# Performance work log

Measured on AMD Instinct MI355X. Metric: run time of the kernel, lower is better.

Reference implementation:

```python
import jax, jax.numpy as jnp
import numpy as np

NUM_SLOTS = 8
DIM = 256
ITERS = 3
EPS_LN = 1e-5

def _ln(x, g, b):
    mu = jnp.mean(x, axis=-1, keepdims=True)
    var = jnp.var(x, axis=-1, keepdims=True)
    return (x - mu) * jax.lax.rsqrt(var + EPS_LN) * g + b

def setup_inputs() -> dict:
    key = jax.random.key(0)
    ks = jax.random.split(key, 16)
    d = DIM
    s = 1.0 / np.sqrt(d)
    inp = {
        'x': jax.random.normal(ks[0], (64, 4096, d), jnp.float32),
        'noise': jax.random.normal(ks[1], (64, NUM_SLOTS, d), jnp.float32),
        'slots_mu': jax.random.normal(ks[2], (1, 1, d), jnp.float32),
        'slots_logsigma': jnp.zeros((1, 1, d), jnp.float32),
        'Wq': jax.random.uniform(ks[3], (d, d), jnp.float32, -s, s),
        'Wk': jax.random.uniform(ks[4], (d, d), jnp.float32, -s, s),
        'Wv': jax.random.uniform(ks[5], (d, d), jnp.float32, -s, s),
        'W_ih': jax.random.uniform(ks[6], (3 * d, d), jnp.float32, -s, s),
        'W_hh': jax.random.uniform(ks[7], (3 * d, d), jnp.float32, -s, s),
        'b_ih': jax.random.uniform(ks[8], (3 * d,), jnp.float32, -s, s),
        'b_hh': jax.random.uniform(ks[9], (3 * d,), jnp.float32, -s, s),
        'W1': jax.random.uniform(ks[10], (d, d), jnp.float32, -s, s),
        'b1': jax.random.uniform(ks[11], (d,), jnp.float32, -s, s),
        'W2': jax.random.uniform(ks[12], (d, d), jnp.float32, -s, s),
        'b2': jax.random.uniform(ks[13], (d,), jnp.float32, -s, s),
        'g_in': jnp.ones((d,), jnp.float32), 'be_in': jnp.zeros((d,), jnp.float32),
        'g_sl': jnp.ones((d,), jnp.float32), 'be_sl': jnp.zeros((d,), jnp.float32),
        'g_ff': jnp.ones((d,), jnp.float32), 'be_ff': jnp.zeros((d,), jnp.float32),
    }
    return inp

def _gru(x, h, W_ih, W_hh, b_ih, b_hh):
    # torch.nn.GRUCell math; x,h: [M, d]
    gi = x @ W_ih.T + b_ih
    gh = h @ W_hh.T + b_hh
    i_r, i_z, i_n = jnp.split(gi, 3, axis=-1)
    h_r, h_z, h_n = jnp.split(gh, 3, axis=-1)
    r = jax.nn.sigmoid(i_r + h_r)
    z = jax.nn.sigmoid(i_z + h_z)
    n = jnp.tanh(i_n + r * h_n)
    return (1.0 - z) * n + z * h

def reference(x, noise, slots_mu, slots_logsigma, Wq, Wk, Wv, W_ih, W_hh, b_ih, b_hh,
              W1, b1, W2, b2, g_in, be_in, g_sl, be_sl, g_ff, be_ff):
    B, N, d = x.shape
    scale = d ** (-0.5)
    x = _ln(x, g_in, be_in)
    slots = slots_mu + noise * jnp.exp(slots_logsigma)  # [B, K, d]
    # k/v are loop-invariant; hoist (same math as original)
    k = jnp.einsum('bnd,ed->bne', x, Wk)
    v = jnp.einsum('bnd,ed->bne', x, Wv)
    for _ in range(ITERS):
        slots_prev = slots
        q = jnp.einsum('bkd,ed->bke', _ln(slots, g_sl, be_sl), Wq)
        attn = jax.nn.softmax(jnp.einsum('bkd,bnd->bkn', q, k) * scale, axis=-1) + 1e-8
        attn = attn / jnp.sum(attn, axis=-1, keepdims=True)
        updates = jnp.einsum('bkn,bnd->bkd', attn, v)
        slots = _gru(updates.reshape(-1, d), slots_prev.reshape(-1, d),
                     W_ih, W_hh, b_ih, b_hh).reshape(B, NUM_SLOTS, d)
        h = jax.nn.relu(jnp.einsum('bkd,ed->bke', _ln(slots, g_ff, be_ff), W1) + b1)
        slots = slots + jnp.einsum('bkd,ed->bke', h, W2) + b2
    return slots.reshape(B, NUM_SLOTS * d)
```

## Files before the change

### kernel.cpp

```cpp
#include <hip/hip_runtime.h>
#include <cstddef>

#define DIM 256
#define NSLOT 8
#define BATCH 64
#define NTOK 4096
#define SEGB 16
#define NPART SEGB
#define ITERS 3
#define EPS 1e-5f

typedef short bf16x8 __attribute__((ext_vector_type(8)));
typedef short bf16x4 __attribute__((ext_vector_type(4)));
typedef float f32x4  __attribute__((ext_vector_type(4)));

static __device__ __forceinline__ short f2bf(float f) {
    union { float f; unsigned u; } v; v.f = f;
    unsigned r = v.u + 0x7fffu + ((v.u >> 16) & 1u);
    return (short)(r >> 16);
}

enum : size_t {
    OFF_M     = 0,
    OFF_WIHT  = OFF_M    + 256 * 256,
    OFF_WHHT  = OFF_WIHT + 256 * 768,
    OFF_WVT   = OFF_WHHT + 256 * 768,
    OFF_W1T   = OFF_WVT  + 256 * 256,
    OFF_W2T   = OFF_W1T  + 256 * 256,
    OFF_SLOTS = OFF_W2T  + 256 * 256,
    OFF_SNEW  = OFF_SLOTS + BATCH * NSLOT * 256,
    OFF_QT    = OFF_SNEW  + BATCH * NSLOT * 256,
    OFF_H     = OFF_QT    + BATCH * NSLOT * 256,
    OFF_UPD   = OFF_H     + BATCH * NSLOT * 256,
    OFF_UPART = OFF_UPD   + BATCH * NSLOT * 256,
    OFF_LPART = OFF_UPART + (size_t)BATCH * NPART * NSLOT * 256,
    WS_FLOATS = OFF_LPART + BATCH * NPART * 16
};

__global__ __launch_bounds__(256) void k_transpose(const float* __restrict__ w_ih,
                                                   const float* __restrict__ w_hh,
                                                   const float* __restrict__ wv,
                                                   const float* __restrict__ w1,
                                                   const float* __restrict__ w2,
                                                   float* __restrict__ ws) {
    int z = blockIdx.z;
    const float* src;
    float* dst;
    int R;
    if (z == 0)      { src = w_ih; dst = ws + OFF_WIHT; R = 768; }
    else if (z == 1) { src = w_hh; dst = ws + OFF_WHHT; R = 768; }
    else if (z == 2) { src = wv;   dst = ws + OFF_WVT;  R = 256; }
    else if (z == 3) { src = w1;   dst = ws + OFF_W1T;  R = 256; }
    else             { src = w2;   dst = ws + OFF_W2T;  R = 256; }
    if ((int)blockIdx.x * 32 >= R) return;
    __shared__ float tile[32][33];
    int lx = threadIdx.x & 31, ly = threadIdx.x >> 5;
    int r0 = blockIdx.x * 32, c0 = blockIdx.y * 32;
#pragma unroll
    for (int p = 0; p < 4; ++p)
        tile[ly + p * 8][lx] = src[(size_t)(r0 + ly + p * 8) * 256 + c0 + lx];
    __syncthreads();
#pragma unroll
    for (int p = 0; p < 4; ++p)
        dst[(size_t)(c0 + ly + p * 8) * R + r0 + lx] = tile[lx][ly + p * 8];
}

__global__ __launch_bounds__(256) void k_m(const float* __restrict__ wq,
                                           const float* __restrict__ wk,
                                           float* __restrict__ ws) {
    int d = blockIdx.x, t = threadIdx.x;
    float acc = 0.f;
    for (int e = 0; e < 256; ++e)
        acc += wq[e * 256 + d] * wk[e * 256 + t];
    ws[OFF_M + d * 256 + t] = acc * 0.0625f;
}

__global__ __launch_bounds__(256) void k_init(const float* __restrict__ mu,
                                              const float* __restrict__ logsig,
                                              const float* __restrict__ noise,
                                              float* __restrict__ ws) {
    int i = blockIdx.x * 256 + threadIdx.x;
    int d = i & 255;
    ws[OFF_SLOTS + i] = mu[d] + noise[i] * __expf(logsig[d]);
}

__global__ __launch_bounds__(256) void k_qt(float* __restrict__ ws,
                                            const float* __restrict__ g_sl,
                                            const float* __restrict__ be_sl) {
    __shared__ float ln[2048];
    int chunk = blockIdx.x, b = blockIdx.y;
    int t = threadIdx.x, wave = t >> 6, lane = t & 63;
    const float* slots = ws + OFF_SLOTS + b * 2048;
    float4 gf = ((const float4*)g_sl)[lane];
    float4 bf = ((const float4*)be_sl)[lane];
#pragma unroll
    for (int rr = 0; rr < 2; ++rr) {
        int r = wave + rr * 4;
        float4 v = ((const float4*)(slots + r * 256))[lane];
        float s1 = v.x + v.y + v.z + v.w;
        float s2 = v.x * v.x + v.y * v.y + v.z * v.z + v.w * v.w;
#pragma unroll
        for (int m = 1; m < 64; m <<= 1) { s1 += __shfl_xor(s1, m); s2 += __shfl_xor(s2, m); }
        float mu = s1 * (1.f / 256.f);
        float rstd = rsqrtf(s2 * (1.f / 256.f) - mu * mu + EPS);
        float4 o;
        o.x = (v.x - mu) * rstd * gf.x + bf.x;
        o.y = (v.y - mu) * rstd * gf.y + bf.y;
        o.z = (v.z - mu) * rstd * gf.z + bf.z;
        o.w = (v.w - mu) * rstd * gf.w + bf.w;
        *((float4*)&ln[r * 256 + lane * 4]) = o;
    }
    __syncthreads();
    const float* M = ws + OFF_M;
    int k0 = t >> 6;
    int e = chunk * 64 + (t & 63);
    float a0 = 0.f, a1 = 0.f;
    for (int d = 0; d < 256; ++d) {
        float m = M[d * 256 + e];
        a0 += ln[k0 * 256 + d] * m;
        a1 += ln[(k0 + 4) * 256 + d] * m;
    }
    float* qt = ws + OFF_QT + b * 2048;
    qt[k0 * 256 + e] = a0;
    qt[(k0 + 4) * 256 + e] = a1;
}

__global__ __launch_bounds__(256) void k_attn(const float* __restrict__ x,
                                              const float* __restrict__ g_in,
                                              const float* __restrict__ be_in,
                                              float* __restrict__ ws) {
    int seg = blockIdx.x, b = blockIdx.y;
    int t = threadIdx.x;
    int w = t >> 6, lane = t & 63;
    int q = lane >> 4, s16 = lane & 15;

    __shared__ short qhi[16 * 264];
    __shared__ short xT[256 * 64];
    __shared__ short Etmp[16 * 72];
    __shared__ float GsL[16], CsL[16];
    __shared__ float lsum[4][8], b1sLDS[4][8];

    const float* qtg = ws + OFF_QT + b * 2048;

    for (int idx = t; idx < 16 * 264; idx += 256) {
        int s = idx / 264, d = idx - s * 264;
        float v = (s < 8 && d < 256) ? qtg[s * 256 + d] * g_in[d] : 0.f;
        qhi[idx] = f2bf(v);
    }
    {
        if (t >= 8 && t < 16) { GsL[t] = 0.f; CsL[t] = 0.f; }
        int s = t >> 5, j = t & 31;
        float pg = 0.f, pc = 0.f;
        for (int d = j; d < 256; d += 32) {
            float qv = qtg[s * 256 + d];
            pg += qv * g_in[d];
            pc += qv * be_in[d];
        }
#pragma unroll
        for (int m = 1; m < 32; m <<= 1) { pg += __shfl_xor(pg, m); pc += __shfl_xor(pc, m); }
        if (j == 0) { GsL[s] = pg; CsL[s] = pc; }
    }
    __syncthreads();

    bf16x8 qf[8];
#pragma unroll
    for (int i = 0; i < 8; ++i)
        qf[i] = *(const bf16x8*)&qhi[s16 * 264 + i * 32 + q * 8];

    float Gv = GsL[s16], Cv = CsL[s16];

    f32x4 U[4];
#pragma unroll
    for (int c = 0; c < 4; ++c) U[c] = (f32x4){0.f, 0.f, 0.f, 0.f};
    float lacc = 0.f, b1acc = 0.f;

    const int tokens_per_block = NTOK / SEGB;
    const int tiles = tokens_per_block / 64;
    int mytok_base = seg * tokens_per_block + w * 16 + s16;
    int g0 = ((w * 16 + s16) >> 3);
    int t7 = s16 & 7;

    for (int tt = 0; tt < tiles; ++tt) {
        const float* xr = x + ((size_t)b * NTOK + (size_t)(mytok_base + tt * 64)) * 256 + q * 8;
        const float4* xp = (const float4*)xr;
        float4 xa[8], xb[8];
#pragma unroll
        for (int i = 0; i < 8; ++i) { xa[i] = xp[8 * i]; xb[i] = xp[8 * i + 1]; }
        float s1 = 0.f, s2 = 0.f;
#pragma unroll
        for (int i = 0; i < 8; ++i) {
            s1 += xa[i].x + xa[i].y + xa[i].z + xa[i].w + xb[i].x + xb[i].y + xb[i].z + xb[i].w;
            s2 += xa[i].x * xa[i].x + xa[i].y * xa[i].y + xa[i].z * xa[i].z + xa[i].w * xa[i].w
                + xb[i].x * xb[i].x + xb[i].y * xb[i].y + xb[i].z * xb[i].z + xb[i].w * xb[i].w;
        }
        s1 += __shfl_xor(s1, 16); s2 += __shfl_xor(s2, 16);
        s1 += __shfl_xor(s1, 32); s2 += __shfl_xor(s2, 32);
        float mu = s1 * (1.f / 256.f);
        float rstd = rsqrtf(s2 * (1.f / 256.f) - mu * mu + EPS);

        bf16x8 af[8];
#pragma unroll
        for (int i = 0; i < 8; ++i) {
            bf16x8 f;
            f[0] = f2bf(xa[i].x); f[1] = f2bf(xa[i].y); f[2] = f2bf(xa[i].z); f[3] = f2bf(xa[i].w);
            f[4] = f2bf(xb[i].x); f[5] = f2bf(xb[i].y); f[6] = f2bf(xb[i].z); f[7] = f2bf(xb[i].w);
            af[i] = f;
        }

        f32x4 Lc = (f32x4){0.f, 0.f, 0.f, 0.f};
#pragma unroll
        for (int i = 0; i < 8; ++i)
            Lc = __builtin_amdgcn_mfma_f32_16x16x32_bf16(af[i], qf[i], Lc, 0, 0, 0);

        float mur[4], rsr[4];
#pragma unroll
        for (int r = 0; r < 4; ++r) {
            mur[r] = __shfl(mu, q * 4 + r);
            rsr[r] = __shfl(rstd, q * 4 + r);
        }
        bf16x4 e2;
#pragma unroll
        for (int r = 0; r < 4; ++r) {
            float logit = rsr[r] * Lc[r] - mur[r] * rsr[r] * Gv + Cv;
            float E = __expf(fminf(logit, 30.f));
            lacc += E;
            b1acc += E * mur[r] * rsr[r];
            e2[r] = f2bf(E * rsr[r]);
        }

        __syncthreads();

#pragma unroll
        for (int i = 0; i < 8; ++i) {
            int Ki = (4 * i + q) & 7;
            int dbase = i * 32 + q * 8;
            bf16x8 f = af[i];
#pragma unroll
            for (int e = 0; e < 8; ++e) {
                int gp = (g0 ^ e ^ Ki) & 7;
                xT[((dbase + e) << 6) + (gp << 3) + t7] = f[e];
            }
        }
        *(bf16x4*)&Etmp[s16 * 72 + w * 16 + q * 4] = e2;

        __syncthreads();

        bf16x8 ea0 = *(const bf16x8*)&Etmp[s16 * 72 + q * 8];
        bf16x8 ea1 = *(const bf16x8*)&Etmp[s16 * 72 + 32 + q * 8];
#pragma unroll
        for (int c = 0; c < 4; ++c) {
            int d = (4 * w + c) * 16 + s16;
            int swz = (d ^ (d >> 3)) & 7;
            const short* row = &xT[d << 6];
            bf16x8 b0 = *(const bf16x8*)&row[((q ^ swz) & 7) << 3];
            bf16x8 b1 = *(const bf16x8*)&row[(((4 + q) ^ swz) & 7) << 3];
            U[c] = __builtin_amdgcn_mfma_f32_16x16x32_bf16(ea0, b0, U[c], 0, 0, 0);
            U[c] = __builtin_amdgcn_mfma_f32_16x16x32_bf16(ea1, b1, U[c], 0, 0, 0);
        }
    }

    lacc += __shfl_xor(lacc, 16); lacc += __shfl_xor(lacc, 32);
    b1acc += __shfl_xor(b1acc, 16); b1acc += __shfl_xor(b1acc, 32);
    __syncthreads();
    if (q == 0 && s16 < 8) { lsum[w][s16] = lacc; b1sLDS[w][s16] = b1acc; }
    __syncthreads();
    float* lpart = ws + OFF_LPART + (size_t)(b * NPART + seg) * 16;
    if (t < 8)  lpart[t] = lsum[0][t] + lsum[1][t] + lsum[2][t] + lsum[3][t];
    if (t >= 8 && t < 16) {
        int s = t - 8;
        lpart[8 + s] = b1sLDS[0][s] + b1sLDS[1][s] + b1sLDS[2][s] + b1sLDS[3][s];
    }
    float* up = ws + OFF_UPART + (size_t)(b * NPART + seg) * NSLOT * 256;
#pragma unroll
    for (int c = 0; c < 4; ++c) {
        int d = (4 * w + c) * 16 + s16;
#pragma unroll
        for (int r = 0; r < 4; ++r) {
            int slot = q * 4 + r;
            if (slot < 8) up[slot * 256 + d] = U[c][r];
        }
    }
}

static __device__ __forceinline__ void ln_row2(const float* src, float* dst,
                                               const float* __restrict__ g,
                                               const float* __restrict__ be,
                                               int wave, int lane) {
    if (wave < 2) {
        float4 v = *(const float4*)(src + wave * 256 + lane * 4);
        float s1 = v.x + v.y + v.z + v.w;
        float s2 = v.x * v.x + v.y * v.y + v.z * v.z + v.w * v.w;
#pragma unroll
        for (int m = 1; m < 64; m <<= 1) { s1 += __shfl_xor(s1, m); s2 += __shfl_xor(s2, m); }
        float mu = s1 * (1.f / 256.f);
        float rstd = rsqrtf(s2 * (1.f / 256.f) - mu * mu + EPS);
        float4 gf = ((const float4*)g)[lane];
        float4 bf = ((const float4*)be)[lane];
        float4 o;
        o.x = (v.x - mu) * rstd * gf.x + bf.x;
        o.y = (v.y - mu) * rstd * gf.y + bf.y;
        o.z = (v.z - mu) * rstd * gf.z + bf.z;
        o.w = (v.w - mu) * rstd * gf.w + bf.w;
        *(float4*)(dst + wave * 256 + lane * 4) = o;
    }
}

__global__ __launch_bounds__(512) void k_fused(float* __restrict__ ws,
                                               const float* __restrict__ g_in,
                                               const float* __restrict__ be_in,
                                               const float* __restrict__ b_ih,
                                               const float* __restrict__ b_hh,
                                               const float* __restrict__ g_ff,
                                               const float* __restrict__ be_ff,
                                               const float* __restrict__ b1p,
                                               const float* __restrict__ b2p,
                                               const float* __restrict__ g_sl,
                                               const float* __restrict__ be_sl,
                                               float* __restrict__ dout) {
    __shared__ __align__(16) float uc[2][256], upd[2][256], sl[2][256], snew[2][256];
    __shared__ __align__(16) float lnb[2][256], hbuf[2][256], so[2][256];
    __shared__ float lsv[2], b1vs[2];

    int sp = blockIdx.x, b = blockIdx.y, t = threadIdx.x;
    int s0 = sp * 2;
    int s = t >> 8, d = t & 255;
    int wave = t >> 6, lane = t & 63;

    if (t < 32) {
        int ss = t >> 4, g = t & 15;
        const float* lp = ws + OFF_LPART + (size_t)(b * NPART + g) * 16;
        float lv = lp[s0 + ss];
        float bv = lp[8 + s0 + ss];
#pragma unroll
        for (int m = 1; m < 16; m <<= 1) { lv += __shfl_xor(lv, m); bv += __shfl_xor(bv, m); }
        if ((t & 15) == 0) { lsv[ss] = lv; b1vs[ss] = bv; }
    }

    const float* up0 = ws + OFF_UPART + (size_t)b * NPART * NSLOT * 256 + (s0 + s) * 256 + d;
    float acc = 0.f;
#pragma unroll
    for (int g = 0; g < NPART; ++g) acc += up0[(size_t)g * NSLOT * 256];
    sl[s][d] = ws[OFF_SLOTS + (size_t)b * 2048 + (s0 + s) * 256 + d];
    __syncthreads();
    {
        float gd = g_in[d], bd = be_in[d];
        uc[s][d] = (gd * (acc - b1vs[s]) + bd * lsv[s]) / lsv[s];
    }
    __syncthreads();

    {
        const float* WvT = ws + OFF_WVT;
        float o = 0.f;
        for (int dd = 0; dd < 256; ++dd) o += uc[s][dd] * WvT[dd * 256 + d];
        upd[s][d] = o;
    }
    __syncthreads();

    {
        const float* WihT = ws + OFF_WIHT;
        const float* WhhT = ws + OFF_WHHT;
        float ar = 0.f, az = 0.f, an = 0.f, hr = 0.f, hz = 0.f, hn = 0.f;
        for (int dd = 0; dd < 256; ++dd) {
            float ud = upd[s][dd], sd = sl[s][dd];
            const float* wi = WihT + dd * 768;
            const float* wh = WhhT + dd * 768;
            ar += ud * wi[d];       az += ud * wi[256 + d]; an += ud * wi[512 + d];
            hr += sd * wh[d];       hz += sd * wh[256 + d]; hn += sd * wh[512 + d];
        }
        float rg = 1.f / (1.f + __expf(-(ar + b_ih[d] + hr + b_hh[d])));
        float zg = 1.f / (1.f + __expf(-(az + b_ih[256 + d] + hz + b_hh[256 + d])));
        float ng = tanhf(an + b_ih[512 + d] + rg * (hn + b_hh[512 + d]));
        snew[s][d] = (1.f - zg) * ng + zg * sl[s][d];
    }
    __syncthreads();

    ln_row2(&snew[0][0], &lnb[0][0], g_ff, be_ff, wave, lane);
    __syncthreads();

    {
        const float* W1T = ws + OFF_W1T;
        float o = 0.f;
        for (int dd = 0; dd < 256; ++dd) o += lnb[s][dd] * W1T[dd * 256 + d];
        hbuf[s][d] = fmaxf(o + b1p[d], 0.f);
    }
    __syncthreads();

    {
        const float* W2T = ws + OFF_W2T;
        float o = 0.f;
        for (int dd = 0; dd < 256; ++dd) o += hbuf[s][dd] * W2T[dd * 256 + d];
        float r = snew[s][d] + o + b2p[d];
        so[s][d] = r;
        ws[OFF_SLOTS + (size_t)b * 2048 + (s0 + s) * 256 + d] = r;
        if (dout) dout[(size_t)b * 2048 + (s0 + s) * 256 + d] = r;
    }

    if (!dout) {
        __syncthreads();
        ln_row2(&so[0][0], &lnb[0][0], g_sl, be_sl, wave, lane);
        __syncthreads();
        const float* M = ws + OFF_M;
        float o = 0.f;
        for (int dd = 0; dd < 256; ++dd) o += lnb[s][dd] * M[dd * 256 + d];
        ws[OFF_QT + (size_t)b * 2048 + (s0 + s) * 256 + d] = o;
    }
}

extern "C" void kernel_launch(void* const* d_in, const int* in_sizes, int n_in,
                              void* d_out, int out_size, void* d_ws, size_t ws_size,
                              hipStream_t stream) {
    const float* x      = (const float*)d_in[0];
    const float* noise  = (const float*)d_in[1];
    const float* mu     = (const float*)d_in[2];
    const float* logsig = (const float*)d_in[3];
    const float* Wq     = (const float*)d_in[4];
    const float* Wk     = (const float*)d_in[5];
    const float* Wv     = (const float*)d_in[6];
    const float* W_ih   = (const float*)d_in[7];
    const float* W_hh   = (const float*)d_in[8];
    const float* b_ih   = (const float*)d_in[9];
    const float* b_hh   = (const float*)d_in[10];
    const float* W1     = (const float*)d_in[11];
    const float* b1     = (const float*)d_in[12];
    const float* W2     = (const float*)d_in[13];
    const float* b2     = (const float*)d_in[14];
    const float* g_in   = (const float*)d_in[15];
    const float* be_in  = (const float*)d_in[16];
    const float* g_sl   = (const float*)d_in[17];
    const float* be_sl  = (const float*)d_in[18];
    const float* g_ff   = (const float*)d_in[19];
    const float* be_ff  = (const float*)d_in[20];
    float* ws = (float*)d_ws;
    float* out = (float*)d_out;

    hipLaunchKernelGGL(k_transpose, dim3(24, 8, 5), dim3(256), 0, stream, W_ih, W_hh, Wv, W1, W2, ws);
    hipLaunchKernelGGL(k_m, dim3(256), dim3(256), 0, stream, Wq, Wk, ws);
    hipLaunchKernelGGL(k_init, dim3(512), dim3(256), 0, stream, mu, logsig, noise, ws);
    hipLaunchKernelGGL(k_qt, dim3(4, 64), dim3(256), 0, stream, ws, g_sl, be_sl);
    for (int it = 0; it < ITERS; ++it) {
        hipLaunchKernelGGL(k_attn, dim3(SEGB, 64), dim3(256), 0, stream, x, g_in, be_in, ws);
        hipLaunchKernelGGL(k_fused, dim3(4, 64), dim3(512), 0, stream, ws, g_in, be_in,
                           b_ih, b_hh, g_ff, be_ff, b1, b2, g_sl, be_sl,
                           (it == ITERS - 1) ? out : nullptr);
    }
}
```

Before: 764.9 us.

## Precompute normalized bf16 x and its transpose once, reuse across iterations

Adds a prep kernel that layer-normalizes x once, converts it to bf16, and writes both a row-major copy and a per-tile transposed copy to workspace. The attention kernel then reads these bf16 tiles instead of re-reading fp32 x, recomputing LN statistics, and transposing through LDS on every one of the three iterations. The LN affine folding (G/C corrections and the b1 partial sums) is dropped and the fused kernel simplifies accordingly. The trade is extra workspace (two bf16 copies of x) and one extra pass that writes them, in exchange for halving per-iteration read bytes and removing per-iteration conversion and LDS transpose work.

New measurement: 837.1 us. 9.4% more time.

```diff
diff --git a/kernel.cpp b/kernel.cpp
--- a/kernel.cpp
+++ b/kernel.cpp
@@ -34,7 +34,9 @@
     OFF_UPD   = OFF_H     + BATCH * NSLOT * 256,
     OFF_UPART = OFF_UPD   + BATCH * NSLOT * 256,
     OFF_LPART = OFF_UPART + (size_t)BATCH * NPART * NSLOT * 256,
-    WS_FLOATS = OFF_LPART + BATCH * NPART * 16
+    OFF_XLN   = OFF_LPART + BATCH * NPART * 16,
+    OFF_XLT   = OFF_XLN   + (size_t)BATCH * NTOK * 128,
+    WS_FLOATS = OFF_XLT   + (size_t)BATCH * NTOK * 128
 };
 
 __global__ __launch_bounds__(256) void k_transpose(const float* __restrict__ w_ih,
@@ -84,6 +86,98 @@
     ws[OFF_SLOTS + i] = mu[d] + noise[i] * __expf(logsig[d]);
 }
 
+__global__ __launch_bounds__(256) void k_prep(const float* __restrict__ x,
+                                              const float* __restrict__ g_in,
+                                              const float* __restrict__ be_in,
+                                              float* __restrict__ ws) {
+    int seg = blockIdx.x, b = blockIdx.y;
+    int t = threadIdx.x;
+    int w = t >> 6, lane = t & 63;
+    int q = lane >> 4, s16 = lane & 15;
+
+    __shared__ short xT[256 * 64];
+    __shared__ float gl[256], bl[256];
+    gl[t] = g_in[t];
+    bl[t] = be_in[t];
+    __syncthreads();
+
+    short* xln = (short*)(ws + OFF_XLN);
+    short* xlt = (short*)(ws + OFF_XLT);
+    int g0 = ((w * 16 + s16) >> 3);
+    int t7 = s16 & 7;
+
+    for (int tt = 0; tt < 4; ++tt) {
+        int tok = seg * 256 + tt * 64 + w * 16 + s16;
+        const float4* xp = (const float4*)(x + ((size_t)b * NTOK + tok) * 256 + q * 8);
+        float4 xa[8], xb[8];
+#pragma unroll
+        for (int i = 0; i < 8; ++i) { xa[i] = xp[8 * i]; xb[i] = xp[8 * i + 1]; }
+        float s1 = 0.f, s2 = 0.f;
+#pragma unroll
+        for (int i = 0; i < 8; ++i) {
+            s1 += xa[i].x + xa[i].y + xa[i].z + xa[i].w + xb[i].x + xb[i].y + xb[i].z + xb[i].w;
+            s2 += xa[i].x * xa[i].x + xa[i].y * xa[i].y + xa[i].z * xa[i].z + xa[i].w * xa[i].w
+                + xb[i].x * xb[i].x + xb[i].y * xb[i].y + xb[i].z * xb[i].z + xb[i].w * xb[i].w;
+        }
+        s1 += __shfl_xor(s1, 16); s2 += __shfl_xor(s2, 16);
+        s1 += __shfl_xor(s1, 32); s2 += __shfl_xor(s2, 32);
+        float mu = s1 * (1.f / 256.f);
+        float rstd = rsqrtf(s2 * (1.f / 256.f) - mu * mu + EPS);
+
+        bf16x8 af[8];
+#pragma unroll
+        for (int i = 0; i < 8; ++i) {
+            int dbase = i * 32 + q * 8;
+            float4 gA = *(const float4*)&gl[dbase];
+            float4 gB = *(const float4*)&gl[dbase + 4];
+            float4 bA = *(const float4*)&bl[dbase];
+            float4 bB = *(const float4*)&bl[dbase + 4];
+            bf16x8 f;
+            f[0] = f2bf((xa[i].x - mu) * rstd * gA.x + bA.x);
+            f[1] = f2bf((xa[i].y - mu) * rstd * gA.y + bA.y);
+            f[2] = f2bf((xa[i].z - mu) * rstd * gA.z + bA.z);
+            f[3] = f2bf((xa[i].w - mu) * rstd * gA.w + bA.w);
+            f[4] = f2bf((xb[i].x - mu) * rstd * gB.x + bB.x);
+            f[5] = f2bf((xb[i].y - mu) * rstd * gB.y + bB.y);
+            f[6] = f2bf((xb[i].z - mu) * rstd * gB.z + bB.z);
+            f[7] = f2bf((xb[i].w - mu) * rstd * gB.w + bB.w);
+            af[i] = f;
+        }
+
+        short* xrow = xln + ((size_t)b * NTOK + tok) * 256;
+#pragma unroll
+        for (int i = 0; i < 8; ++i)
+            *(bf16x8*)&xrow[i * 32 + q * 8] = af[i];
+
+        __syncthreads();
+
+#pragma unroll
+        for (int i = 0; i < 8; ++i) {
+            int Ki = (4 * i + q) & 7;
+            int dbase = i * 32 + q * 8;
+            bf16x8 f = af[i];
+#pragma unroll
+            for (int e = 0; e < 8; ++e) {
+                int gp = (g0 ^ e ^ Ki) & 7;
+                xT[((dbase + e) << 6) + (gp << 3) + t7] = f[e];
+            }
+        }
+        __syncthreads();
+
+        short* xtb = xlt + (size_t)(b * 64 + seg * 4 + tt) * 256 * 64;
+#pragma unroll
+        for (int c = 0; c < 4; ++c) {
+            int d = (4 * w + c) * 16 + s16;
+            int swz = (d ^ (d >> 3)) & 7;
+            const short* row = &xT[d << 6];
+            bf16x8 b0 = *(const bf16x8*)&row[((q ^ swz) & 7) << 3];
+            bf16x8 b1 = *(const bf16x8*)&row[(((4 + q) ^ swz) & 7) << 3];
+            *(bf16x8*)&xtb[d * 64 + q * 8] = b0;
+            *(bf16x8*)&xtb[d * 64 + (q + 4) * 8] = b1;
+        }
+    }
+}
+
 __global__ __launch_bounds__(256) void k_qt(float* __restrict__ ws,
                                             const float* __restrict__ g_sl,
                                             const float* __restrict__ be_sl) {
@@ -125,40 +219,20 @@
     qt[(k0 + 4) * 256 + e] = a1;
 }
 
-__global__ __launch_bounds__(256) void k_attn(const float* __restrict__ x,
-                                              const float* __restrict__ g_in,
-                                              const float* __restrict__ be_in,
-                                              float* __restrict__ ws) {
+__global__ __launch_bounds__(256) void k_attn(float* __restrict__ ws) {
     int seg = blockIdx.x, b = blockIdx.y;
     int t = threadIdx.x;
     int w = t >> 6, lane = t & 63;
     int q = lane >> 4, s16 = lane & 15;
 
     __shared__ short qhi[16 * 264];
-    __shared__ short xT[256 * 64];
-    __shared__ short Etmp[16 * 72];
-    __shared__ float GsL[16], CsL[16];
-    __shared__ float lsum[4][8], b1sLDS[4][8];
+    __shared__ short Etmp[2][16 * 72];
+    __shared__ float lsum[4][8];
 
     const float* qtg = ws + OFF_QT + b * 2048;
-
     for (int idx = t; idx < 16 * 264; idx += 256) {
         int s = idx / 264, d = idx - s * 264;
-        float v = (s < 8 && d < 256) ? qtg[s * 256 + d] * g_in[d] : 0.f;
-        qhi[idx] = f2bf(v);
-    }
-    {
-        if (t >= 8 && t < 16) { GsL[t] = 0.f; CsL[t] = 0.f; }
-        int s = t >> 5, j = t & 31;
-        float pg = 0.f, pc = 0.f;
-        for (int d = j; d < 256; d += 32) {
-            float qv = qtg[s * 256 + d];
-            pg += qv * g_in[d];
-            pc += qv * be_in[d];
-        }
-#pragma unroll
-        for (int m = 1; m < 32; m <<= 1) { pg += __shfl_xor(pg, m); pc += __shfl_xor(pc, m); }
-        if (j == 0) { GsL[s] = pg; CsL[s] = pc; }
+        qhi[idx] = (s < 8 && d < 256) ? f2bf(qtg[s * 256 + d]) : (short)0;
     }
     __syncthreads();
 
@@ -167,109 +241,56 @@
     for (int i = 0; i < 8; ++i)
         qf[i] = *(const bf16x8*)&qhi[s16 * 264 + i * 32 + q * 8];
 
-    float Gv = GsL[s16], Cv = CsL[s16];
-
     f32x4 U[4];
 #pragma unroll
     for (int c = 0; c < 4; ++c) U[c] = (f32x4){0.f, 0.f, 0.f, 0.f};
-    float lacc = 0.f, b1acc = 0.f;
-
-    const int tokens_per_block = NTOK / SEGB;
-    const int tiles = tokens_per_block / 64;
-    int mytok_base = seg * tokens_per_block + w * 16 + s16;
-    int g0 = ((w * 16 + s16) >> 3);
-    int t7 = s16 & 7;
-
-    for (int tt = 0; tt < tiles; ++tt) {
-        const float* xr = x + ((size_t)b * NTOK + (size_t)(mytok_base + tt * 64)) * 256 + q * 8;
-        const float4* xp = (const float4*)xr;
-        float4 xa[8], xb[8];
-#pragma unroll
-        for (int i = 0; i < 8; ++i) { xa[i] = xp[8 * i]; xb[i] = xp[8 * i + 1]; }
-        float s1 = 0.f, s2 = 0.f;
-#pragma unroll
-        for (int i = 0; i < 8; ++i) {
-            s1 += xa[i].x + xa[i].y + xa[i].z + xa[i].w + xb[i].x + xb[i].y + xb[i].z + xb[i].w;
-            s2 += xa[i].x * xa[i].x + xa[i].y * xa[i].y + xa[i].z * xa[i].z + xa[i].w * xa[i].w
-                + xb[i].x * xb[i].x + xb[i].y * xb[i].y + xb[i].z * xb[i].z + xb[i].w * xb[i].w;
-        }
-        s1 += __shfl_xor(s1, 16); s2 += __shfl_xor(s2, 16);
-        s1 += __shfl_xor(s1, 32); s2 += __shfl_xor(s2, 32);
-        float mu = s1 * (1.f / 256.f);
-        float rstd = rsqrtf(s2 * (1.f / 256.f) - mu * mu + EPS);
-
+    float lacc = 0.f;
+
+    const short* xln = (const short*)(ws + OFF_XLN);
+    const short* xlt = (const short*)(ws + OFF_XLT);
+    int mytok = seg * 256 + w * 16 + s16;
+
+    for (int tt = 0; tt < 4; ++tt) {
+        const short* xr = xln + ((size_t)b * NTOK + mytok + tt * 64) * 256 + q * 8;
         bf16x8 af[8];
 #pragma unroll
-        for (int i = 0; i < 8; ++i) {
-            bf16x8 f;
-            f[0] = f2bf(xa[i].x); f[1] = f2bf(xa[i].y); f[2] = f2bf(xa[i].z); f[3] = f2bf(xa[i].w);
-            f[4] = f2bf(xb[i].x); f[5] = f2bf(xb[i].y); f[6] = f2bf(xb[i].z); f[7] = f2bf(xb[i].w);
-            af[i] = f;
-        }
+        for (int i = 0; i < 8; ++i) af[i] = *(const bf16x8*)&xr[i * 32];
 
         f32x4 Lc = (f32x4){0.f, 0.f, 0.f, 0.f};
 #pragma unroll
         for (int i = 0; i < 8; ++i)
             Lc = __builtin_amdgcn_mfma_f32_16x16x32_bf16(af[i], qf[i], Lc, 0, 0, 0);
 
-        float mur[4], rsr[4];
+        bf16x4 e2;
 #pragma unroll
         for (int r = 0; r < 4; ++r) {
-            mur[r] = __shfl(mu, q * 4 + r);
-            rsr[r] = __shfl(rstd, q * 4 + r);
-        }
-        bf16x4 e2;
-#pragma unroll
-        for (int r = 0; r < 4; ++r) {
-            float logit = rsr[r] * Lc[r] - mur[r] * rsr[r] * Gv + Cv;
-            float E = __expf(fminf(logit, 30.f));
+            float E = __expf(fminf(Lc[r], 30.f));
             lacc += E;
-            b1acc += E * mur[r] * rsr[r];
-            e2[r] = f2bf(E * rsr[r]);
-        }
-
+            e2[r] = f2bf(E);
+        }
+        *(bf16x4*)&Etmp[tt & 1][s16 * 72 + w * 16 + q * 4] = e2;
         __syncthreads();
 
-#pragma unroll
-        for (int i = 0; i < 8; ++i) {
-            int Ki = (4 * i + q) & 7;
-            int dbase = i * 32 + q * 8;
-            bf16x8 f = af[i];
-#pragma unroll
-            for (int e = 0; e < 8; ++e) {
-                int gp = (g0 ^ e ^ Ki) & 7;
-                xT[((dbase + e) << 6) + (gp << 3) + t7] = f[e];
-            }
-        }
-        *(bf16x4*)&Etmp[s16 * 72 + w * 16 + q * 4] = e2;
-
-        __syncthreads();
-
-        bf16x8 ea0 = *(const bf16x8*)&Etmp[s16 * 72 + q * 8];
-        bf16x8 ea1 = *(const bf16x8*)&Etmp[s16 * 72 + 32 + q * 8];
+        bf16x8 ea0 = *(const bf16x8*)&Etmp[tt & 1][s16 * 72 + q * 8];
+        bf16x8 ea1 = *(const bf16x8*)&Etmp[tt & 1][s16 * 72 + 32 + q * 8];
+
+        const short* xtb = xlt + (size_t)(b * 64 + seg * 4 + tt) * 256 * 64;
 #pragma unroll
         for (int c = 0; c < 4; ++c) {
             int d = (4 * w + c) * 16 + s16;
-            int swz = (d ^ (d >> 3)) & 7;
-            const short* row = &xT[d << 6];
-            bf16x8 b0 = *(const bf16x8*)&row[((q ^ swz) & 7) << 3];
-            bf16x8 b1 = *(const bf16x8*)&row[(((4 + q) ^ swz) & 7) << 3];
+            bf16x8 b0 = *(const bf16x8*)&xtb[d * 64 + q * 8];
+            bf16x8 b1 = *(const bf16x8*)&xtb[d * 64 + (q + 4) * 8];
             U[c] = __builtin_amdgcn_mfma_f32_16x16x32_bf16(ea0, b0, U[c], 0, 0, 0);
             U[c] = __builtin_amdgcn_mfma_f32_16x16x32_bf16(ea1, b1, U[c], 0, 0, 0);
         }
     }
 
     lacc += __shfl_xor(lacc, 16); lacc += __shfl_xor(lacc, 32);
-    b1acc += __shfl_xor(b1acc, 16); b1acc += __shfl_xor(b1acc, 32);
-    __syncthreads();
-    if (q == 0 && s16 < 8) { lsum[w][s16] = lacc; b1sLDS[w][s16] = b1acc; }
+    __syncthreads();
+    if (q == 0 && s16 < 8) lsum[w][s16] = lacc;
     __syncthreads();
     float* lpart = ws + OFF_LPART + (size_t)(b * NPART + seg) * 16;
-    if (t < 8)  lpart[t] = lsum[0][t] + lsum[1][t] + lsum[2][t] + lsum[3][t];
-    if (t >= 8 && t < 16) {
-        int s = t - 8;
-        lpart[8 + s] = b1sLDS[0][s] + b1sLDS[1][s] + b1sLDS[2][s] + b1sLDS[3][s];
-    }
+    if (t < 8) lpart[t] = lsum[0][t] + lsum[1][t] + lsum[2][t] + lsum[3][t];
     float* up = ws + OFF_UPART + (size_t)(b * NPART + seg) * NSLOT * 256;
 #pragma unroll
     for (int c = 0; c < 4; ++c) {
@@ -306,8 +327,6 @@
 }
 
 __global__ __launch_bounds__(512) void k_fused(float* __restrict__ ws,
-                                               const float* __restrict__ g_in,
-                                               const float* __restrict__ be_in,
                                                const float* __restrict__ b_ih,
                                                const float* __restrict__ b_hh,
                                                const float* __restrict__ g_ff,
@@ -319,7 +338,7 @@
                                                float* __restrict__ dout) {
     __shared__ __align__(16) float uc[2][256], upd[2][256], sl[2][256], snew[2][256];
     __shared__ __align__(16) float lnb[2][256], hbuf[2][256], so[2][256];
-    __shared__ float lsv[2], b1vs[2];
+    __shared__ float lsv[2];
 
     int sp = blockIdx.x, b = blockIdx.y, t = threadIdx.x;
     int s0 = sp * 2;
@@ -328,12 +347,10 @@
 
     if (t < 32) {
         int ss = t >> 4, g = t & 15;
-        const float* lp = ws + OFF_LPART + (size_t)(b * NPART + g) * 16;
-        float lv = lp[s0 + ss];
-        float bv = lp[8 + s0 + ss];
-#pragma unroll
-        for (int m = 1; m < 16; m <<= 1) { lv += __shfl_xor(lv, m); bv += __shfl_xor(bv, m); }
-        if ((t & 15) == 0) { lsv[ss] = lv; b1vs[ss] = bv; }
+        float lv = ws[OFF_LPART + (size_t)(b * NPART + g) * 16 + s0 + ss];
+#pragma unroll
+        for (int m = 1; m < 16; m <<= 1) lv += __shfl_xor(lv, m);
+        if ((t & 15) == 0) lsv[ss] = lv;
     }
 
     const float* up0 = ws + OFF_UPART + (size_t)b * NPART * NSLOT * 256 + (s0 + s) * 256 + d;
@@ -342,10 +359,7 @@
     for (int g = 0; g < NPART; ++g) acc += up0[(size_t)g * NSLOT * 256];
     sl[s][d] = ws[OFF_SLOTS + (size_t)b * 2048 + (s0 + s) * 256 + d];
     __syncthreads();
-    {
-        float gd = g_in[d], bd = be_in[d];
-        uc[s][d] = (gd * (acc - b1vs[s]) + bd * lsv[s]) / lsv[s];
-    }
+    uc[s][d] = acc / lsv[s];
     __syncthreads();
 
     {
@@ -436,10 +450,11 @@
     hipLaunchKernelGGL(k_transpose, dim3(24, 8, 5), dim3(256), 0, stream, W_ih, W_hh, Wv, W1, W2, ws);
     hipLaunchKernelGGL(k_m, dim3(256), dim3(256), 0, stream, Wq, Wk, ws);
     hipLaunchKernelGGL(k_init, dim3(512), dim3(256), 0, stream, mu, logsig, noise, ws);
+    hipLaunchKernelGGL(k_prep, dim3(SEGB, 64), dim3(256), 0, stream, x, g_in, be_in, ws);
     hipLaunchKernelGGL(k_qt, dim3(4, 64), dim3(256), 0, stream, ws, g_sl, be_sl);
     for (int it = 0; it < ITERS; ++it) {
-        hipLaunchKernelGGL(k_attn, dim3(SEGB, 64), dim3(256), 0, stream, x, g_in, be_in, ws);
-        hipLaunchKernelGGL(k_fused, dim3(4, 64), dim3(512), 0, stream, ws, g_in, be_in,
+        hipLaunchKernelGGL(k_attn, dim3(SEGB, 64), dim3(256), 0, stream, ws);
+        hipLaunchKernelGGL(k_fused, dim3(4, 64), dim3(512), 0, stream, ws,
                            b_ih, b_hh, g_ff, be_ff, b1, b2, g_sl, be_sl,
                            (it == ITERS - 1) ? out : nullptr);
     }
```
